# Performance work log

Hardware: AMD Instinct MI355X
Metric: run time of the kernel (lower is better)

## Reference

```python
import jax, jax.numpy as jnp
import numpy as np

N = 500_000   # total nodes in batched graph
E = 10_000_000  # total edges
G = 1_000     # number of graphs in the batch
H = 8         # hidden_dim
C = 8         # n_classes


def setup_inputs() -> dict:
    key = jax.random.key(0)
    k1, k2, k3, k4, k5, k6 = jax.random.split(key, 6)
    src = jax.random.randint(k1, (E,), 0, N)
    dst = jax.random.randint(k2, (E,), 0, N)
    graph_ids = jnp.sort(jax.random.randint(k3, (N,), 0, G))
    W1 = jax.random.normal(k4, (1, H), dtype=jnp.float32) * 0.5
    W2 = jax.random.normal(k5, (H, H), dtype=jnp.float32) * 0.3
    Wlast = jax.random.normal(k6, (H, C), dtype=jnp.float32) * 0.3
    return {"W1": W1, "W2": W2, "Wlast": Wlast,
            "src": src, "dst": dst, "graph_ids": graph_ids}


def reference(W1, W2, Wlast, src, dst, graph_ids):
    ones_e = jnp.ones(src.shape[0], dtype=jnp.float32)
    deg_in = jax.ops.segment_sum(ones_e, dst, num_segments=N)   # in-degrees
    deg_out = jax.ops.segment_sum(ones_e, src, num_segments=N)  # out-degrees
    # DGL GraphConv norm='both': clamp degrees to >=1, then pow(-1/2)
    inv_sqrt_out = jnp.maximum(deg_out, 1.0) ** -0.5
    inv_sqrt_in = jnp.maximum(deg_in, 1.0) ** -0.5

    def gconv(h, W):
        # h: [N, d]; gather-scatter message passing, then dense transform
        h = h * inv_sqrt_out[:, None]
        agg = jax.ops.segment_sum(h[src], dst, num_segments=N)
        return (agg * inv_sqrt_in[:, None]) @ W

    h = deg_in[:, None]  # input feature = in_degrees, shape [N, 1]
    h = jax.nn.relu(gconv(h, W1))
    h = jax.nn.relu(gconv(h, W2))

    # dgl.mean_nodes: per-graph mean over nodes
    counts = jax.ops.segment_sum(jnp.ones(N, dtype=jnp.float32), graph_ids,
                                 num_segments=G)
    hg = jax.ops.segment_sum(h, graph_ids, num_segments=G)
    hg = hg / jnp.maximum(counts, 1.0)[:, None]
    return hg @ Wlast  # [G, n_classes], Linear with bias=False
```

## Files before the change

### kernel.cpp

```cpp
#include <hip/hip_runtime.h>


#define TB 256
#define STB 512
#define BSH 13
#define BNODES 8192
#define MAXNB 64
#define SCH 4096
#define SCH4 (SCH / 4)
#define EPT 8
#define CSTR 16
#define INVB 0xFFFFFFFFu

__global__ void init_kernel(unsigned* __restrict__ curD, unsigned* __restrict__ curS,
                            float* __restrict__ Xsum, int NB, unsigned CAP, int G) {
    int i = blockIdx.x * TB + threadIdx.x;
    if (i < NB) { curD[i * CSTR] = (unsigned)i * CAP; curS[i * CSTR] = (unsigned)i * CAP; }
    if (i < G) Xsum[i] = 0.0f;
}

__global__ void scatter_sort_kernel(const int* __restrict__ src, const int* __restrict__ dst,
                                    unsigned* __restrict__ curD, unsigned* __restrict__ curS,
                                    unsigned* __restrict__ dstP, unsigned short* __restrict__ srcP,
                                    int NB, int E) {
    __shared__ unsigned cntD[MAXNB], cntS[MAXNB];
    __shared__ unsigned deltaD[MAXNB], deltaS[MAXNB];
    __shared__ unsigned totD_s, totS_s;
    __shared__ unsigned payD[SCH];
    __shared__ unsigned short valS[SCH];
    __shared__ unsigned char mapD[SCH], mapS[SCH];

    int tid = threadIdx.x;
    if (tid < MAXNB) { cntD[tid] = 0u; cntS[tid] = 0u; }
    __syncthreads();

    unsigned sA[EPT], dA[EPT], bD[EPT], bS[EPT];
    int blk = blockIdx.x;
#pragma unroll
    for (int v = 0; v < 2; ++v) {
        int q = blk * SCH4 + v * STB + tid;
        int be = q * 4;
        if (be + 3 < E) {
            int4 s4 = ((const int4*)src)[q];
            int4 d4 = ((const int4*)dst)[q];
            sA[v*4+0] = (unsigned)s4.x; sA[v*4+1] = (unsigned)s4.y;
            sA[v*4+2] = (unsigned)s4.z; sA[v*4+3] = (unsigned)s4.w;
            dA[v*4+0] = (unsigned)d4.x; dA[v*4+1] = (unsigned)d4.y;
            dA[v*4+2] = (unsigned)d4.z; dA[v*4+3] = (unsigned)d4.w;
#pragma unroll
            for (int k = 0; k < 4; ++k) {
                bD[v*4+k] = dA[v*4+k] >> BSH;
                bS[v*4+k] = sA[v*4+k] >> BSH;
            }
        } else {
#pragma unroll
            for (int k = 0; k < 4; ++k) {
                int j = be + k;
                if (j < E) {
                    sA[v*4+k] = (unsigned)src[j];
                    dA[v*4+k] = (unsigned)dst[j];
                    bD[v*4+k] = dA[v*4+k] >> BSH;
                    bS[v*4+k] = sA[v*4+k] >> BSH;
                } else {
                    bD[v*4+k] = INVB; bS[v*4+k] = INVB;
                    sA[v*4+k] = 0u; dA[v*4+k] = 0u;
                }
            }
        }
    }

#pragma unroll
    for (int k = 0; k < EPT; ++k) {
        if (bD[k] != INVB) {
            atomicAdd(&cntD[bD[k]], 1u);
            atomicAdd(&cntS[bS[k]], 1u);
        }
    }
    __syncthreads();

    int wv = tid >> 6, ln = tid & 63;
    if (wv == 0) {
        unsigned x = (ln < NB) ? cntD[ln] : 0u;
        unsigned inc = x;
#pragma unroll
        for (int o = 1; o < 64; o <<= 1) {
            unsigned y = __shfl_up(inc, o, 64);
            if (ln >= o) inc += y;
        }
        unsigned exc = inc - x;
        if (ln < NB) {
            unsigned gb = atomicAdd(&curD[ln * CSTR], x);
            deltaD[ln] = gb - exc;
            cntD[ln] = exc;
        }
        if (ln == 63) totD_s = inc;
    } else if (wv == 1) {
        unsigned x = (ln < NB) ? cntS[ln] : 0u;
        unsigned inc = x;
#pragma unroll
        for (int o = 1; o < 64; o <<= 1) {
            unsigned y = __shfl_up(inc, o, 64);
            if (ln >= o) inc += y;
        }
        unsigned exc = inc - x;
        if (ln < NB) {
            unsigned gb = atomicAdd(&curS[ln * CSTR], x);
            deltaS[ln] = gb - exc;
            cntS[ln] = exc;
        }
        if (ln == 63) totS_s = inc;
    }
    __syncthreads();

#pragma unroll
    for (int k = 0; k < EPT; ++k) {
        if (bD[k] != INVB) {
            unsigned p = atomicAdd(&cntD[bD[k]], 1u);
            payD[p] = ((dA[k] & (BNODES - 1)) << 19) | sA[k];
            mapD[p] = (unsigned char)bD[k];
            unsigned p2 = atomicAdd(&cntS[bS[k]], 1u);
            valS[p2] = (unsigned short)(sA[k] & (BNODES - 1));
            mapS[p2] = (unsigned char)bS[k];
        }
    }
    __syncthreads();

    unsigned tD = totD_s, tS = totS_s;
    for (unsigned i = tid; i < tD; i += STB) {
        unsigned b = mapD[i];
        dstP[deltaD[b] + i] = payD[i];
    }
    for (unsigned i = tid; i < tS; i += STB) {
        unsigned b = mapS[i];
        srcP[deltaS[b] + i] = valS[i];
    }
}

__global__ void deghist_kernel(const unsigned short* __restrict__ srcP, const unsigned* __restrict__ dstP,
                               const unsigned* __restrict__ curS, const unsigned* __restrict__ curD,
                               unsigned CAP, unsigned* __restrict__ pDeg, int Jlg) {
    __shared__ unsigned h[BNODES];
    for (int t = threadIdx.x; t < BNODES; t += TB) h[t] = 0u;
    __syncthreads();
    int b = blockIdx.x >> Jlg;
    int j = blockIdx.x & ((1 << Jlg) - 1);
    unsigned s0 = (unsigned)b * CAP;
    unsigned cD = curD[b * CSTR] - s0;
    unsigned lo = (unsigned)(((unsigned long long)cD * (unsigned)j) >> Jlg);
    unsigned hi = (unsigned)(((unsigned long long)cD * (unsigned)(j + 1)) >> Jlg);
    for (unsigned i = lo + threadIdx.x; i < hi; i += TB)
        atomicAdd(&h[dstP[s0 + i] >> 19], 0x10000u);
    unsigned cS = curS[b * CSTR] - s0;
    lo = (unsigned)(((unsigned long long)cS * (unsigned)j) >> Jlg);
    hi = (unsigned)(((unsigned long long)cS * (unsigned)(j + 1)) >> Jlg);
    for (unsigned i = lo + threadIdx.x; i < hi; i += TB)
        atomicAdd(&h[srcP[s0 + i]], 1u);
    __syncthreads();
    unsigned* row = pDeg + (size_t)blockIdx.x * BNODES;
    for (int t = threadIdx.x; t < BNODES; t += TB) row[t] = h[t];
}

__global__ void prep_kernel(const unsigned* __restrict__ pDeg,
                            float* __restrict__ pio, float* __restrict__ h0s,
                            float* __restrict__ isiA, int Jlg, int Npad) {
    int i = blockIdx.x * TB + threadIdx.x;
    if (i >= Npad) return;
    int b = i >> BSH, l = i & (BNODES - 1);
    int J = 1 << Jlg;
    unsigned sum = 0;
    for (int j = 0; j < J; ++j)
        sum += pDeg[(size_t)((b << Jlg) + j) * BNODES + l];
    float din = (float)(sum >> 16), dout = (float)(sum & 0xFFFFu);
    float a  = 1.0f / sqrtf(fmaxf(din, 1.0f));
    float bo = 1.0f / sqrtf(fmaxf(dout, 1.0f));
    pio[i]  = a * bo;
    h0s[i]  = din * bo;
    isiA[i] = a;
}

__global__ void wh_kernel(const unsigned* __restrict__ dstP, const unsigned* __restrict__ curD,
                          unsigned CAP, const float* __restrict__ table,
                          float* __restrict__ pOut, int Jlg) {
    __shared__ float h[BNODES];
    for (int t = threadIdx.x; t < BNODES; t += TB) h[t] = 0.0f;
    __syncthreads();
    int b = blockIdx.x >> Jlg;
    int j = blockIdx.x & ((1 << Jlg) - 1);
    unsigned s0 = (unsigned)b * CAP;
    unsigned cD = curD[b * CSTR] - s0;
    unsigned lo = (unsigned)(((unsigned long long)cD * (unsigned)j) >> Jlg);
    unsigned hi = (unsigned)(((unsigned long long)cD * (unsigned)(j + 1)) >> Jlg);
    for (unsigned i = lo + threadIdx.x; i < hi; i += TB) {
        unsigned e = dstP[s0 + i];
        atomicAdd(&h[e >> 19], table[e & 0x7FFFFu]);
    }
    __syncthreads();
    float* row = pOut + (size_t)blockIdx.x * BNODES;
    for (int t = threadIdx.x; t < BNODES; t += TB) row[t] = h[t];
}

__global__ void mid_kernel(const float* __restrict__ pC, const float* __restrict__ pio,
                           float* __restrict__ sarr, int Jlg, int Npad) {
    int i = blockIdx.x * TB + threadIdx.x;
    if (i >= Npad) return;
    int b = i >> BSH, l = i & (BNODES - 1);
    int J = 1 << Jlg;
    float t1 = 0.0f;
    for (int j = 0; j < J; ++j)
        t1 += pC[(size_t)((b << Jlg) + j) * BNODES + l];
    sarr[i] = t1 * pio[i];
}

__global__ void poolfinal_kernel(const float* __restrict__ pT, const float* __restrict__ isiA,
                                 const int* __restrict__ graph_ids,
                                 float* __restrict__ Xsum, int Jlg, int N) {
    int i = blockIdx.x * TB + threadIdx.x;
    bool valid = i < N;
    int ii = valid ? i : (N - 1);
    int b = ii >> BSH, l = ii & (BNODES - 1);
    int J = 1 << Jlg;
    float t2 = 0.0f;
    for (int j = 0; j < J; ++j)
        t2 += pT[(size_t)((b << Jlg) + j) * BNODES + l];
    float x = valid ? t2 * isiA[ii] : 0.0f;
    int g = graph_ids[ii];
    int g0 = __shfl(g, 0, 64);
    bool uniform = __all((!valid) || (g == g0));
    if (uniform) {
#pragma unroll
        for (int off = 32; off >= 1; off >>= 1) x += __shfl_down(x, off, 64);
        if ((threadIdx.x & 63) == 0) atomicAdd(&Xsum[g0], x);
    } else if (valid) {
        atomicAdd(&Xsum[g], x);
    }
}

__global__ void final_kernel(const float* __restrict__ Xsum, const int* __restrict__ graph_ids,
                             const float* __restrict__ W1, const float* __restrict__ W2,
                             const float* __restrict__ Wlast,
                             float* __restrict__ out, int N, int GC) {
    int i = blockIdx.x * TB + threadIdx.x;
    if (i < GC) {
        int g = i >> 3, j = i & 7;
        int lo = 0, hi = N;
        while (lo < hi) { int m = (lo + hi) >> 1; if (graph_ids[m] < g) lo = m + 1; else hi = m; }
        int lo2 = lo, hi2 = N;
        while (lo2 < hi2) { int m = (lo2 + hi2) >> 1; if (graph_ids[m] < g + 1) lo2 = m + 1; else hi2 = m; }
        float c = (float)(lo2 - lo);
        float r = 0.0f;
#pragma unroll
        for (int cc = 0; cc < 8; ++cc) {
            float m = 0.0f;
#pragma unroll
            for (int k = 0; k < 8; ++k) m += fmaxf(W1[k], 0.0f) * W2[k * 8 + cc];
            r += fmaxf(m, 0.0f) * Wlast[cc * 8 + j];
        }
        out[i] = Xsum[g] / fmaxf(c, 1.0f) * r;
    }
}


__global__ void fb_deg_kernel(const int* __restrict__ src, const int* __restrict__ dst,
                              float* __restrict__ deg_out, float* __restrict__ deg_in, int E) {
    int i = blockIdx.x * TB + threadIdx.x;
    if (i < E) {
        atomicAdd(&deg_out[src[i]], 1.0f);
        atomicAdd(&deg_in[dst[i]], 1.0f);
    }
}

__global__ void fb_prep_kernel(const float* __restrict__ deg_in, const float* __restrict__ deg_out,
                               float* __restrict__ isi, float* __restrict__ iso,
                               float* __restrict__ h0s, int N) {
    int i = blockIdx.x * TB + threadIdx.x;
    if (i < N) {
        float di = deg_in[i], dn = deg_out[i];
        float a = 1.0f / sqrtf(fmaxf(di, 1.0f));
        float b = 1.0f / sqrtf(fmaxf(dn, 1.0f));
        isi[i] = a; iso[i] = b; h0s[i] = di * b;
    }
}

__global__ void fb_conv_kernel(const int* __restrict__ src, const int* __restrict__ dst,
                               const float* __restrict__ vals, float* __restrict__ t, int E) {
    int i = blockIdx.x * TB + threadIdx.x;
    if (i < E) atomicAdd(&t[dst[i]], vals[src[i]]);
}

__global__ void fb_mid_kernel(const float* __restrict__ agg1, const float* __restrict__ isi,
                              const float* __restrict__ iso, float* __restrict__ s, int N) {
    int i = blockIdx.x * TB + threadIdx.x;
    if (i < N) s[i] = agg1[i] * isi[i] * iso[i];
}

__global__ void fb_pool_kernel(const float* __restrict__ t2, const float* __restrict__ isi,
                               const int* __restrict__ graph_ids,
                               float* __restrict__ Xsum, float* __restrict__ counts, int N) {
    int i = blockIdx.x * TB + threadIdx.x;
    bool valid = i < N;
    int ii = valid ? i : (N - 1);
    float x = valid ? t2[ii] * isi[ii] : 0.0f;
    float cnt = valid ? 1.0f : 0.0f;
    int g = graph_ids[ii];
    int g0 = __shfl(g, 0, 64);
    bool uniform = __all((!valid) || (g == g0));
    if (uniform) {
#pragma unroll
        for (int off = 32; off >= 1; off >>= 1) {
            x += __shfl_down(x, off, 64);
            cnt += __shfl_down(cnt, off, 64);
        }
        if ((threadIdx.x & 63) == 0) { atomicAdd(&Xsum[g0], x); atomicAdd(&counts[g0], cnt); }
    } else if (valid) {
        atomicAdd(&Xsum[g], x); atomicAdd(&counts[g], 1.0f);
    }
}

__global__ void fb_final_kernel(const float* __restrict__ Xsum, const float* __restrict__ counts,
                                const float* __restrict__ W1, const float* __restrict__ W2,
                                const float* __restrict__ Wlast, float* __restrict__ out, int GC) {
    int i = blockIdx.x * TB + threadIdx.x;
    if (i < GC) {
        int g = i >> 3, j = i & 7;
        float r = 0.0f;
#pragma unroll
        for (int c = 0; c < 8; ++c) {
            float m = 0.0f;
#pragma unroll
            for (int k = 0; k < 8; ++k) m += fmaxf(W1[k], 0.0f) * W2[k * 8 + c];
            r += fmaxf(m, 0.0f) * Wlast[c * 8 + j];
        }
        out[i] = Xsum[g] / fmaxf(counts[g], 1.0f) * r;
    }
}


extern "C" void kernel_launch(void* const* d_in, const int* in_sizes, int n_in,
                              void* d_out, int out_size, void* d_ws, size_t ws_size,
                              hipStream_t stream) {
    const float* W1        = (const float*)d_in[0];
    const float* W2        = (const float*)d_in[1];
    const float* Wlast     = (const float*)d_in[2];
    const int*   src       = (const int*)d_in[3];
    const int*   dst       = (const int*)d_in[4];
    const int*   graph_ids = (const int*)d_in[5];
    float* out = (float*)d_out;

    const int E = in_sizes[3];
    const int N = in_sizes[5];
    const int G = out_size / 8;

    int NB   = (N + BNODES - 1) >> BSH;
    int Npad = NB << BSH;
    int NCH  = (E + SCH - 1) / SCH;
    unsigned CAP = (unsigned)(((E / (NB > 0 ? NB : 1)) + 8192 + 511) & ~511);

    int Jlg = 3;
    size_t req = 0;
    size_t o_dstP, o_srcP, o_curD, o_curS, o_part, o_pio, o_h0sar, o_isi, o_Xsum;
    for (;; --Jlg) {
        int J = 1 << Jlg;
        size_t off = 0;
        auto A = [&](size_t bytes) { size_t o = off; off = (off + bytes + 127) & ~(size_t)127; return o; };
        o_dstP  = A((size_t)NB * CAP * 4);
        o_srcP  = A((size_t)NB * CAP * 2);
        o_curD  = A((size_t)NB * CSTR * 4);
        o_curS  = A((size_t)NB * CSTR * 4);
        o_part  = A((size_t)NB * J * BNODES * 4);
        o_pio   = A((size_t)Npad * 4);
        o_h0sar = A((size_t)Npad * 4);
        o_isi   = A((size_t)Npad * 4);
        o_Xsum  = A((size_t)G * 4);
        req = off;
        if (req <= ws_size || Jlg == 0) break;
    }

    bool fast = (N <= (1 << 19)) && (NB <= MAXNB) && (ws_size >= req) && (E >= 1);

    char* bp = (char*)d_ws;

    if (fast) {
        unsigned*       dstP = (unsigned*)(bp + o_dstP);
        unsigned short* srcP = (unsigned short*)(bp + o_srcP);
        unsigned* curD = (unsigned*)(bp + o_curD);
        unsigned* curS = (unsigned*)(bp + o_curS);
        unsigned* pDeg = (unsigned*)(bp + o_part);
        float*    pC   = (float*)(bp + o_part);
        float*    pT   = (float*)(bp + o_part);
        float* pio  = (float*)(bp + o_pio);
        float* h0s  = (float*)(bp + o_h0sar);
        float* sarr = (float*)(bp + o_h0sar);
        float* isiA = (float*)(bp + o_isi);
        float* Xsum = (float*)(bp + o_Xsum);

        int gridNp = (Npad + TB - 1) / TB;
        int gridN  = (N + TB - 1) / TB;
        int J = 1 << Jlg;
        int gridI = (max(NB, G) + TB - 1) / TB;

        init_kernel<<<gridI, TB, 0, stream>>>(curD, curS, Xsum, NB, CAP, G);
        scatter_sort_kernel<<<NCH, STB, 0, stream>>>(src, dst, curD, curS, dstP, srcP, NB, E);
        deghist_kernel<<<NB * J, TB, 0, stream>>>(srcP, dstP, curS, curD, CAP, pDeg, Jlg);
        prep_kernel<<<gridNp, TB, 0, stream>>>(pDeg, pio, h0s, isiA, Jlg, Npad);
        wh_kernel<<<NB * J, TB, 0, stream>>>(dstP, curD, CAP, h0s, pC, Jlg);
        mid_kernel<<<gridNp, TB, 0, stream>>>(pC, pio, sarr, Jlg, Npad);
        wh_kernel<<<NB * J, TB, 0, stream>>>(dstP, curD, CAP, sarr, pT, Jlg);
        poolfinal_kernel<<<gridN, TB, 0, stream>>>(pT, isiA, graph_ids, Xsum, Jlg, N);
        final_kernel<<<(out_size + TB - 1) / TB, TB, 0, stream>>>(Xsum, graph_ids,
                                                                  W1, W2, Wlast, out, N, out_size);
    } else {
        float* ws = (float*)d_ws;
        size_t f = 0;
        auto FA = [&](size_t n) { size_t o = f; f += (n + 3) & ~(size_t)3; return o; };
        size_t f_degin  = FA(N);
        size_t f_degout = FA(N);
        size_t f_agg1   = FA(N);
        size_t f_t2     = FA(N);
        size_t f_Xsum   = FA(G);
        size_t f_cnt    = FA(G);
        size_t zf = f;
        size_t f_isi = FA(N);
        size_t f_iso = FA(N);
        size_t f_h0s = FA(N);
        size_t f_s   = FA(N);
        hipMemsetAsync(ws, 0, zf * sizeof(float), stream);
        int gridE = (E + TB - 1) / TB;
        int gridN = (N + TB - 1) / TB;
        int gridO = (out_size + TB - 1) / TB;
        fb_deg_kernel<<<gridE, TB, 0, stream>>>(src, dst, ws + f_degout, ws + f_degin, E);
        fb_prep_kernel<<<gridN, TB, 0, stream>>>(ws + f_degin, ws + f_degout,
                                                 ws + f_isi, ws + f_iso, ws + f_h0s, N);
        fb_conv_kernel<<<gridE, TB, 0, stream>>>(src, dst, ws + f_h0s, ws + f_agg1, E);
        fb_mid_kernel<<<gridN, TB, 0, stream>>>(ws + f_agg1, ws + f_isi, ws + f_iso, ws + f_s, N);
        fb_conv_kernel<<<gridE, TB, 0, stream>>>(src, dst, ws + f_s, ws + f_t2, E);
        fb_pool_kernel<<<gridN, TB, 0, stream>>>(ws + f_t2, ws + f_isi, graph_ids,
                                                 ws + f_Xsum, ws + f_cnt, N);
        fb_final_kernel<<<gridO, TB, 0, stream>>>(ws + f_Xsum, ws + f_cnt, W1, W2, Wlast,
                                                  out, out_size);
    }
}
```

Measured before the change: 391.5 us.

## Compute degrees with global atomics instead of a second source bucket sort

Drops the source-side bucket scatter, the srcP array and the deghist kernel. In-degree and out-degree are now counted with global atomicAdd on per-node counters directly inside the scatter kernel, and prep reads those counters instead of reducing partial histograms. This removes a full sort pass over the edges, a kernel launch and the partial histogram traffic. In exchange it issues 20M random global atomics spread over 500K nodes, which may contend or be slow on the device.

```diff
diff --git a/kernel.cpp b/kernel.cpp
--- a/kernel.cpp
+++ b/kernel.cpp
@@ -12,29 +12,31 @@
 #define CSTR 16
 #define INVB 0xFFFFFFFFu
 
-__global__ void init_kernel(unsigned* __restrict__ curD, unsigned* __restrict__ curS,
-                            float* __restrict__ Xsum, int NB, unsigned CAP, int G) {
-    int i = blockIdx.x * TB + threadIdx.x;
-    if (i < NB) { curD[i * CSTR] = (unsigned)i * CAP; curS[i * CSTR] = (unsigned)i * CAP; }
+__global__ void init_kernel(unsigned* __restrict__ curD, float* __restrict__ Xsum,
+                            unsigned* __restrict__ degD, unsigned* __restrict__ degS,
+                            int NB, unsigned CAP, int G, int Npad) {
+    int i = blockIdx.x * TB + threadIdx.x;
+    if (i < NB) curD[i * CSTR] = (unsigned)i * CAP;
     if (i < G) Xsum[i] = 0.0f;
+    if (i < Npad) { degD[i] = 0u; degS[i] = 0u; }
 }
 
 __global__ void scatter_sort_kernel(const int* __restrict__ src, const int* __restrict__ dst,
-                                    unsigned* __restrict__ curD, unsigned* __restrict__ curS,
-                                    unsigned* __restrict__ dstP, unsigned short* __restrict__ srcP,
+                                    unsigned* __restrict__ curD,
+                                    unsigned* __restrict__ dstP,
+                                    unsigned* __restrict__ degD, unsigned* __restrict__ degS,
                                     int NB, int E) {
-    __shared__ unsigned cntD[MAXNB], cntS[MAXNB];
-    __shared__ unsigned deltaD[MAXNB], deltaS[MAXNB];
-    __shared__ unsigned totD_s, totS_s;
+    __shared__ unsigned cntD[MAXNB];
+    __shared__ unsigned deltaD[MAXNB];
+    __shared__ unsigned totD_s;
     __shared__ unsigned payD[SCH];
-    __shared__ unsigned short valS[SCH];
-    __shared__ unsigned char mapD[SCH], mapS[SCH];
+    __shared__ unsigned char mapD[SCH];
 
     int tid = threadIdx.x;
-    if (tid < MAXNB) { cntD[tid] = 0u; cntS[tid] = 0u; }
-    __syncthreads();
-
-    unsigned sA[EPT], dA[EPT], bD[EPT], bS[EPT];
+    if (tid < MAXNB) cntD[tid] = 0u;
+    __syncthreads();
+
+    unsigned sA[EPT], dA[EPT], bD[EPT];
     int blk = blockIdx.x;
 #pragma unroll
     for (int v = 0; v < 2; ++v) {
@@ -48,10 +50,7 @@
             dA[v*4+0] = (unsigned)d4.x; dA[v*4+1] = (unsigned)d4.y;
             dA[v*4+2] = (unsigned)d4.z; dA[v*4+3] = (unsigned)d4.w;
 #pragma unroll
-            for (int k = 0; k < 4; ++k) {
-                bD[v*4+k] = dA[v*4+k] >> BSH;
-                bS[v*4+k] = sA[v*4+k] >> BSH;
-            }
+            for (int k = 0; k < 4; ++k) bD[v*4+k] = dA[v*4+k] >> BSH;
         } else {
 #pragma unroll
             for (int k = 0; k < 4; ++k) {
@@ -60,9 +59,8 @@
                     sA[v*4+k] = (unsigned)src[j];
                     dA[v*4+k] = (unsigned)dst[j];
                     bD[v*4+k] = dA[v*4+k] >> BSH;
-                    bS[v*4+k] = sA[v*4+k] >> BSH;
                 } else {
-                    bD[v*4+k] = INVB; bS[v*4+k] = INVB;
+                    bD[v*4+k] = INVB;
                     sA[v*4+k] = 0u; dA[v*4+k] = 0u;
                 }
             }
@@ -72,9 +70,14 @@
 #pragma unroll
     for (int k = 0; k < EPT; ++k) {
         if (bD[k] != INVB) {
-            atomicAdd(&cntD[bD[k]], 1u);
-            atomicAdd(&cntS[bS[k]], 1u);
-        }
+            atomicAdd(&degD[dA[k]], 1u);
+            atomicAdd(&degS[sA[k]], 1u);
+        }
+    }
+
+#pragma unroll
+    for (int k = 0; k < EPT; ++k) {
+        if (bD[k] != INVB) atomicAdd(&cntD[bD[k]], 1u);
     }
     __syncthreads();
 
@@ -94,21 +97,6 @@
             cntD[ln] = exc;
         }
         if (ln == 63) totD_s = inc;
-    } else if (wv == 1) {
-        unsigned x = (ln < NB) ? cntS[ln] : 0u;
-        unsigned inc = x;
-#pragma unroll
-        for (int o = 1; o < 64; o <<= 1) {
-            unsigned y = __shfl_up(inc, o, 64);
-            if (ln >= o) inc += y;
-        }
-        unsigned exc = inc - x;
-        if (ln < NB) {
-            unsigned gb = atomicAdd(&curS[ln * CSTR], x);
-            deltaS[ln] = gb - exc;
-            cntS[ln] = exc;
-        }
-        if (ln == 63) totS_s = inc;
     }
     __syncthreads();
 
@@ -118,59 +106,23 @@
             unsigned p = atomicAdd(&cntD[bD[k]], 1u);
             payD[p] = ((dA[k] & (BNODES - 1)) << 19) | sA[k];
             mapD[p] = (unsigned char)bD[k];
-            unsigned p2 = atomicAdd(&cntS[bS[k]], 1u);
-            valS[p2] = (unsigned short)(sA[k] & (BNODES - 1));
-            mapS[p2] = (unsigned char)bS[k];
-        }
-    }
-    __syncthreads();
-
-    unsigned tD = totD_s, tS = totS_s;
+        }
+    }
+    __syncthreads();
+
+    unsigned tD = totD_s;
     for (unsigned i = tid; i < tD; i += STB) {
         unsigned b = mapD[i];
         dstP[deltaD[b] + i] = payD[i];
     }
-    for (unsigned i = tid; i < tS; i += STB) {
-        unsigned b = mapS[i];
-        srcP[deltaS[b] + i] = valS[i];
-    }
-}
-
-__global__ void deghist_kernel(const unsigned short* __restrict__ srcP, const unsigned* __restrict__ dstP,
-                               const unsigned* __restrict__ curS, const unsigned* __restrict__ curD,
-                               unsigned CAP, unsigned* __restrict__ pDeg, int Jlg) {
-    __shared__ unsigned h[BNODES];
-    for (int t = threadIdx.x; t < BNODES; t += TB) h[t] = 0u;
-    __syncthreads();
-    int b = blockIdx.x >> Jlg;
-    int j = blockIdx.x & ((1 << Jlg) - 1);
-    unsigned s0 = (unsigned)b * CAP;
-    unsigned cD = curD[b * CSTR] - s0;
-    unsigned lo = (unsigned)(((unsigned long long)cD * (unsigned)j) >> Jlg);
-    unsigned hi = (unsigned)(((unsigned long long)cD * (unsigned)(j + 1)) >> Jlg);
-    for (unsigned i = lo + threadIdx.x; i < hi; i += TB)
-        atomicAdd(&h[dstP[s0 + i] >> 19], 0x10000u);
-    unsigned cS = curS[b * CSTR] - s0;
-    lo = (unsigned)(((unsigned long long)cS * (unsigned)j) >> Jlg);
-    hi = (unsigned)(((unsigned long long)cS * (unsigned)(j + 1)) >> Jlg);
-    for (unsigned i = lo + threadIdx.x; i < hi; i += TB)
-        atomicAdd(&h[srcP[s0 + i]], 1u);
-    __syncthreads();
-    unsigned* row = pDeg + (size_t)blockIdx.x * BNODES;
-    for (int t = threadIdx.x; t < BNODES; t += TB) row[t] = h[t];
-}
-
-__global__ void prep_kernel(const unsigned* __restrict__ pDeg,
+}
+
+__global__ void prep_kernel(const unsigned* __restrict__ degD, const unsigned* __restrict__ degS,
                             float* __restrict__ pio, float* __restrict__ h0s,
-                            float* __restrict__ isiA, int Jlg, int Npad) {
+                            float* __restrict__ isiA, int Npad) {
     int i = blockIdx.x * TB + threadIdx.x;
     if (i >= Npad) return;
-    int b = i >> BSH, l = i & (BNODES - 1);
-    int J = 1 << Jlg;
-    unsigned sum = 0;
-    for (int j = 0; j < J; ++j)
-        sum += pDeg[(size_t)((b << Jlg) + j) * BNODES + l];
-    float din = (float)(sum >> 16), dout = (float)(sum & 0xFFFFu);
+    float din = (float)degD[i], dout = (float)degS[i];
     float a  = 1.0f / sqrtf(fmaxf(din, 1.0f));
     float bo = 1.0f / sqrtf(fmaxf(dout, 1.0f));
     pio[i]  = a * bo;
@@ -357,15 +309,15 @@
 
     int Jlg = 3;
     size_t req = 0;
-    size_t o_dstP, o_srcP, o_curD, o_curS, o_part, o_pio, o_h0sar, o_isi, o_Xsum;
+    size_t o_dstP, o_curD, o_degD, o_degS, o_part, o_pio, o_h0sar, o_isi, o_Xsum;
     for (;; --Jlg) {
         int J = 1 << Jlg;
         size_t off = 0;
         auto A = [&](size_t bytes) { size_t o = off; off = (off + bytes + 127) & ~(size_t)127; return o; };
         o_dstP  = A((size_t)NB * CAP * 4);
-        o_srcP  = A((size_t)NB * CAP * 2);
         o_curD  = A((size_t)NB * CSTR * 4);
-        o_curS  = A((size_t)NB * CSTR * 4);
+        o_degD  = A((size_t)Npad * 4);
+        o_degS  = A((size_t)Npad * 4);
         o_part  = A((size_t)NB * J * BNODES * 4);
         o_pio   = A((size_t)Npad * 4);
         o_h0sar = A((size_t)Npad * 4);
@@ -380,11 +332,10 @@
     char* bp = (char*)d_ws;
 
     if (fast) {
-        unsigned*       dstP = (unsigned*)(bp + o_dstP);
-        unsigned short* srcP = (unsigned short*)(bp + o_srcP);
+        unsigned* dstP = (unsigned*)(bp + o_dstP);
         unsigned* curD = (unsigned*)(bp + o_curD);
-        unsigned* curS = (unsigned*)(bp + o_curS);
-        unsigned* pDeg = (unsigned*)(bp + o_part);
+        unsigned* degD = (unsigned*)(bp + o_degD);
+        unsigned* degS = (unsigned*)(bp + o_degS);
         float*    pC   = (float*)(bp + o_part);
         float*    pT   = (float*)(bp + o_part);
         float* pio  = (float*)(bp + o_pio);
@@ -396,12 +347,11 @@
         int gridNp = (Npad + TB - 1) / TB;
         int gridN  = (N + TB - 1) / TB;
         int J = 1 << Jlg;
-        int gridI = (max(NB, G) + TB - 1) / TB;
-
-        init_kernel<<<gridI, TB, 0, stream>>>(curD, curS, Xsum, NB, CAP, G);
-        scatter_sort_kernel<<<NCH, STB, 0, stream>>>(src, dst, curD, curS, dstP, srcP, NB, E);
-        deghist_kernel<<<NB * J, TB, 0, stream>>>(srcP, dstP, curS, curD, CAP, pDeg, Jlg);
-        prep_kernel<<<gridNp, TB, 0, stream>>>(pDeg, pio, h0s, isiA, Jlg, Npad);
+        int gridI = (max(max(NB, G), Npad) + TB - 1) / TB;
+
+        init_kernel<<<gridI, TB, 0, stream>>>(curD, Xsum, degD, degS, NB, CAP, G, Npad);
+        scatter_sort_kernel<<<NCH, STB, 0, stream>>>(src, dst, curD, dstP, degD, degS, NB, E);
+        prep_kernel<<<gridNp, TB, 0, stream>>>(degD, degS, pio, h0s, isiA, Npad);
         wh_kernel<<<NB * J, TB, 0, stream>>>(dstP, curD, CAP, h0s, pC, Jlg);
         mid_kernel<<<gridNp, TB, 0, stream>>>(pC, pio, sarr, Jlg, Npad);
         wh_kernel<<<NB * J, TB, 0, stream>>>(dstP, curD, CAP, sarr, pT, Jlg);
```

New measurement: 1.074 ms. +174.4%, slower.
